# Kernel optimization log

Hardware: AMD Instinct MI355X
Metric: run time of the kernel (lower is better)

Reference implementation:

```python
import jax, jax.numpy as jnp
import numpy as np

N_NODES = 100000
N_EDGES = 1600000
IN_DIM, HID_DIM, OUT_DIM = 64, 64, 16


def setup_inputs() -> dict:
    key = jax.random.key(0)
    k1, k2, k3, k4 = jax.random.split(key, 4)
    x = jax.random.normal(k1, (N_NODES, IN_DIM), dtype=jnp.float32)
    edge_index = jax.random.randint(k2, (2, N_EDGES), 0, N_NODES, dtype=jnp.int64)
    W1 = jax.random.normal(k3, (IN_DIM, HID_DIM), dtype=jnp.float32) * (1.0 / np.sqrt(IN_DIM))
    b1 = jnp.zeros((HID_DIM,), dtype=jnp.float32)
    W2 = jax.random.normal(k4, (HID_DIM, OUT_DIM), dtype=jnp.float32) * (1.0 / np.sqrt(HID_DIM))
    b2 = jnp.zeros((OUT_DIM,), dtype=jnp.float32)
    return {"x": x, "edge_index": edge_index, "W1": W1, "b1": b1, "W2": W2, "b2": b2}


def gcn_conv(x, src, dst, W, b, num_nodes):
    """GCNConv: h = D^{-1/2} (A+I) D^{-1/2} (x W) + b, edge-list form with self-loops already appended."""
    # symmetric degree normalization (degree counted at destination, incl. self-loops)
    deg = jax.ops.segment_sum(jnp.ones_like(dst, dtype=x.dtype), dst, num_segments=num_nodes)
    dinv = jnp.where(deg > 0, jax.lax.rsqrt(deg), 0.0)
    norm = dinv[src] * dinv[dst]                      # [E+N]
    h = x @ W                                         # [N, H] project first (fewer flops on edges)
    msg = h[src] * norm[:, None]                      # gather + scale, [E+N, H]
    out = jax.ops.segment_sum(msg, dst, num_segments=num_nodes)  # scatter-add
    return out + b


def reference(x, edge_index, W1, b1, W2, b2):
    num_nodes = x.shape[0]
    loop = jnp.arange(num_nodes, dtype=edge_index.dtype)
    src = jnp.concatenate([edge_index[0], loop])      # add self-loops once, reuse for both layers
    dst = jnp.concatenate([edge_index[1], loop])
    h = gcn_conv(x, src, dst, W1, b1, num_nodes)
    h = jax.nn.relu(h)
    # F.dropout(training=self.training): eval mode -> identity
    out = gcn_conv(h, src, dst, W2, b2, num_nodes)
    return out
```

## Files before the change

### kernel.cpp

```cpp
#include <hip/hip_runtime.h>

constexpr int N_NODES = 100000;
constexpr int F1 = 64;
constexpr int F2 = 16;
constexpr int SH = 7;
constexpr int NPB = 128;
constexpr int NBINS = (N_NODES + NPB - 1) / NPB;
constexpr int CAPB = 2560;
constexpr int TILE = 4096;

static __device__ __forceinline__ unsigned short f2bf(float f) {
    unsigned int u = __float_as_uint(f);
    unsigned int r = (u + 0x7fffu + ((u >> 16) & 1u)) >> 16;
    return (unsigned short)r;
}
static __device__ __forceinline__ float bf2f(unsigned short b) {
    return __uint_as_float(((unsigned int)b) << 16);
}
static __device__ __forceinline__ float lo16(unsigned int u) { return __uint_as_float(u << 16); }
static __device__ __forceinline__ float hi16(unsigned int u) { return __uint_as_float(u & 0xFFFF0000u); }

__global__ __launch_bounds__(512) void k_bin(const int* __restrict__ src,
                                             const int* __restrict__ dst, int E,
                                             unsigned int* __restrict__ gcnt,
                                             unsigned int* __restrict__ entries) {
    __shared__ unsigned int cnt[NBINS];
    __shared__ unsigned int cur[NBINS];
    int tid = threadIdx.x;
    int base = blockIdx.x * TILE;
    int end = min(base + TILE, E + N_NODES);
    for (int i = tid; i < NBINS; i += 512) cnt[i] = 0;
    __syncthreads();
    for (int e = base + tid; e < end; e += 512) {
        int d = (e < E) ? dst[e] : (e - E);
        atomicAdd(&cnt[d >> SH], 1u);
    }
    __syncthreads();
    for (int i = tid; i < NBINS; i += 512) {
        unsigned int c = cnt[i];
        cur[i] = (unsigned int)i * CAPB + (c ? atomicAdd(&gcnt[i], c) : 0u);
    }
    __syncthreads();
    for (int e = base + tid; e < end; e += 512) {
        int d, s;
        if (e < E) { d = dst[e]; s = src[e]; }
        else       { d = e - E;  s = d; }
        int bb = d >> SH;
        unsigned int p = atomicAdd(&cur[bb], 1u);
        if (p - (unsigned int)bb * CAPB < CAPB)
            entries[p] = (unsigned int)s | ((unsigned int)(d & (NPB - 1)) << 17);
    }
}

__global__ __launch_bounds__(512) void k_csr(const unsigned int* __restrict__ gcnt,
                                             const unsigned int* __restrict__ entries,
                                             uint2* __restrict__ nrange,
                                             unsigned int* __restrict__ sorted,
                                             float* __restrict__ dinv) {
    __shared__ unsigned int ncnt[NPB];
    __shared__ unsigned int noff[NPB + 1];
    __shared__ unsigned int cur[NPB];
    int tid = threadIdx.x;
    int b = blockIdx.x;
    unsigned int cntE = gcnt[b]; if (cntE > CAPB) cntE = CAPB;
    unsigned int base = (unsigned int)b * CAPB;
    if (tid < NPB) ncnt[tid] = 0;
    __syncthreads();
    for (unsigned int e = tid; e < cntE; e += 512)
        atomicAdd(&ncnt[entries[base + e] >> 17], 1u);
    __syncthreads();
    if (tid < NPB) cur[tid] = ncnt[tid];
    __syncthreads();
    for (int ofs = 1; ofs < NPB; ofs <<= 1) {
        unsigned int v = (tid < NPB && tid >= ofs) ? cur[tid - ofs] : 0u;
        __syncthreads();
        if (tid < NPB) cur[tid] += v;
        __syncthreads();
    }
    if (tid < NPB) noff[tid + 1] = cur[tid];
    if (tid == 0) noff[0] = 0;
    __syncthreads();
    if (tid < NPB) {
        int node = b * NPB + tid;
        if (node < N_NODES) {
            dinv[node] = rsqrtf((float)max(ncnt[tid], 1u));
            nrange[node] = make_uint2(base + noff[tid], base + noff[tid + 1]);
        }
        cur[tid] = noff[tid];
    }
    __syncthreads();
    for (unsigned int e = tid; e < cntE; e += 512) {
        unsigned int v = entries[base + e];
        unsigned int p = atomicAdd(&cur[v >> 17], 1u);
        sorted[base + p] = v & 0x1FFFFu;
    }
}

__global__ __launch_bounds__(256) void k_xw1(const float* __restrict__ x,
                                             const float* __restrict__ W,
                                             const float* __restrict__ dinv,
                                             unsigned short* __restrict__ hs) {
    constexpr int XS = 68;
    __shared__ float Ws[64 * 64];
    __shared__ float xs[64 * XS];
    int tid = threadIdx.x;
    int r0 = blockIdx.x * 64;
    for (int i = tid; i < 1024; i += 256) {
        int k = i >> 4, c4 = (i & 15) << 2;
        *(float4*)&Ws[k * 64 + c4] = *(const float4*)&W[k * 64 + c4];
    }
    for (int i = tid; i < 1024; i += 256) {
        int rr = i >> 4, c4 = (i & 15) << 2;
        int r = r0 + rr;
        float4 v = make_float4(0.f, 0.f, 0.f, 0.f);
        if (r < N_NODES) v = *(const float4*)&x[(size_t)r * 64 + c4];
        *(float4*)&xs[rr * XS + c4] = v;
    }
    __syncthreads();
    int tx = tid & 15, ty = tid >> 4;
    int c0 = tx << 2, rb = ty << 2;
    float acc[4][4] = {};
#pragma unroll 8
    for (int k = 0; k < 64; ++k) {
        float4 w = *(float4*)&Ws[k * 64 + c0];
        float x0 = xs[(rb + 0) * XS + k];
        float x1 = xs[(rb + 1) * XS + k];
        float x2 = xs[(rb + 2) * XS + k];
        float x3 = xs[(rb + 3) * XS + k];
        acc[0][0] += x0 * w.x; acc[0][1] += x0 * w.y; acc[0][2] += x0 * w.z; acc[0][3] += x0 * w.w;
        acc[1][0] += x1 * w.x; acc[1][1] += x1 * w.y; acc[1][2] += x1 * w.z; acc[1][3] += x1 * w.w;
        acc[2][0] += x2 * w.x; acc[2][1] += x2 * w.y; acc[2][2] += x2 * w.z; acc[2][3] += x2 * w.w;
        acc[3][0] += x3 * w.x; acc[3][1] += x3 * w.y; acc[3][2] += x3 * w.z; acc[3][3] += x3 * w.w;
    }
#pragma unroll
    for (int i = 0; i < 4; ++i) {
        int r = r0 + rb + i;
        if (r >= N_NODES) break;
        float dv = dinv[r];
        ushort4 p;
        p.x = f2bf(acc[i][0] * dv);
        p.y = f2bf(acc[i][1] * dv);
        p.z = f2bf(acc[i][2] * dv);
        p.w = f2bf(acc[i][3] * dv);
        *(ushort4*)&hs[(size_t)r * 64 + c0] = p;
    }
}

__global__ __launch_bounds__(256) void k_agg1f(const uint2* __restrict__ nrange,
                                               const unsigned int* __restrict__ sorted,
                                               const unsigned short* __restrict__ hs,
                                               const float* __restrict__ dinv,
                                               unsigned short* __restrict__ out1) {
    int gw = (blockIdx.x * 256 + threadIdx.x) >> 6;
    if (gw >= N_NODES) return;
    int lane = threadIdx.x & 63;
    int slot = lane >> 4, t = lane & 15;
    const uint2* hs8 = (const uint2*)hs;
    uint2 rg = nrange[gw];
    float a0 = 0.f, a1 = 0.f, a2 = 0.f, a3 = 0.f;
    for (unsigned int j = rg.x; j < rg.y; j += 64) {
        unsigned int cnt = rg.y - j; if (cnt > 64u) cnt = 64u;
        unsigned int idx = (unsigned)lane < cnt ? sorted[j + lane] : 0u;
        unsigned int rounds = (cnt + 3u) >> 2;
#pragma unroll 4
        for (unsigned int r = 0; r < rounds; ++r) {
            unsigned int sl = (r << 2) + (unsigned)slot;
            unsigned int myidx = (unsigned int)__shfl((int)idx, (int)sl);
            if (sl < cnt) {
                uint2 u = hs8[(size_t)myidx * 16 + t];
                a0 += lo16(u.x); a1 += hi16(u.x);
                a2 += lo16(u.y); a3 += hi16(u.y);
            }
        }
    }
    a0 += __shfl_xor(a0, 16); a1 += __shfl_xor(a1, 16);
    a2 += __shfl_xor(a2, 16); a3 += __shfl_xor(a3, 16);
    a0 += __shfl_xor(a0, 32); a1 += __shfl_xor(a1, 32);
    a2 += __shfl_xor(a2, 32); a3 += __shfl_xor(a3, 32);
    if (slot == 0) {
        float dv = dinv[gw];
        uint2 w;
        w.x = (unsigned)f2bf(a0 * dv) | ((unsigned)f2bf(a1 * dv) << 16);
        w.y = (unsigned)f2bf(a2 * dv) | ((unsigned)f2bf(a3 * dv) << 16);
        ((uint2*)out1)[(size_t)gw * 16 + t] = w;
    }
}

__global__ __launch_bounds__(256) void k_xw2(const unsigned short* __restrict__ out1,
                                             const float* __restrict__ b1,
                                             const float* __restrict__ W2,
                                             const float* __restrict__ dinv,
                                             unsigned short* __restrict__ h2s) {
    constexpr int RS = 66;
    __shared__ float Ws[64 * 16];
    __shared__ float rs[128 * RS];
    __shared__ float b1s[64];
    int tid = threadIdx.x;
    int r0 = blockIdx.x * 128;
    if (tid < 64) b1s[tid] = b1[tid];
    for (int i = tid; i < 256; i += 256)
        *(float4*)&Ws[i * 4] = *(const float4*)&W2[i * 4];
    __syncthreads();
    for (int i = tid; i < 2048; i += 256) {
        int rr = i >> 4, c4 = (i & 15) << 2;
        int r = r0 + rr;
        float v0 = 0.f, v1 = 0.f, v2 = 0.f, v3 = 0.f;
        if (r < N_NODES) {
            ushort4 u = *(const ushort4*)&out1[(size_t)r * 64 + c4];
            v0 = fmaxf(bf2f(u.x) + b1s[c4 + 0], 0.f);
            v1 = fmaxf(bf2f(u.y) + b1s[c4 + 1], 0.f);
            v2 = fmaxf(bf2f(u.z) + b1s[c4 + 2], 0.f);
            v3 = fmaxf(bf2f(u.w) + b1s[c4 + 3], 0.f);
        }
        float* pp = &rs[rr * RS + c4];
        pp[0] = v0; pp[1] = v1; pp[2] = v2; pp[3] = v3;
    }
    __syncthreads();
    int tx = tid & 3, ty = tid >> 2;
    int c0 = tx << 2, rb = ty << 1;
    float acc[2][4] = {};
#pragma unroll 8
    for (int k = 0; k < 64; ++k) {
        float4 w = *(float4*)&Ws[k * 16 + c0];
        float x0 = rs[(rb + 0) * RS + k];
        float x1 = rs[(rb + 1) * RS + k];
        acc[0][0] += x0 * w.x; acc[0][1] += x0 * w.y; acc[0][2] += x0 * w.z; acc[0][3] += x0 * w.w;
        acc[1][0] += x1 * w.x; acc[1][1] += x1 * w.y; acc[1][2] += x1 * w.z; acc[1][3] += x1 * w.w;
    }
#pragma unroll
    for (int i = 0; i < 2; ++i) {
        int r = r0 + rb + i;
        if (r >= N_NODES) break;
        float dv = dinv[r];
        ushort4 p;
        p.x = f2bf(acc[i][0] * dv);
        p.y = f2bf(acc[i][1] * dv);
        p.z = f2bf(acc[i][2] * dv);
        p.w = f2bf(acc[i][3] * dv);
        *(ushort4*)&h2s[(size_t)r * 16 + c0] = p;
    }
}

__global__ __launch_bounds__(256) void k_agg2f(const uint2* __restrict__ nrange,
                                               const unsigned int* __restrict__ sorted,
                                               const unsigned short* __restrict__ h2s,
                                               const float* __restrict__ dinv,
                                               const float* __restrict__ b2,
                                               float* __restrict__ out) {
    int gw = (blockIdx.x * 256 + threadIdx.x) >> 6;
    if (gw >= N_NODES) return;
    int lane = threadIdx.x & 63;
    int slot = lane >> 3, t = lane & 7;
    const unsigned int* h232 = (const unsigned int*)h2s;
    uint2 rg = nrange[gw];
    float a0 = 0.f, a1 = 0.f;
    for (unsigned int j = rg.x; j < rg.y; j += 64) {
        unsigned int cnt = rg.y - j; if (cnt > 64u) cnt = 64u;
        unsigned int idx = (unsigned)lane < cnt ? sorted[j + lane] : 0u;
        unsigned int rounds = (cnt + 7u) >> 3;
#pragma unroll 4
        for (unsigned int r = 0; r < rounds; ++r) {
            unsigned int sl = (r << 3) + (unsigned)slot;
            unsigned int myidx = (unsigned int)__shfl((int)idx, (int)sl);
            if (sl < cnt) {
                unsigned int u = h232[(size_t)myidx * 8 + t];
                a0 += lo16(u);
                a1 += hi16(u);
            }
        }
    }
    a0 += __shfl_xor(a0, 8);  a1 += __shfl_xor(a1, 8);
    a0 += __shfl_xor(a0, 16); a1 += __shfl_xor(a1, 16);
    a0 += __shfl_xor(a0, 32); a1 += __shfl_xor(a1, 32);
    if (slot == 0) {
        float dv = dinv[gw];
        float2 o;
        o.x = a0 * dv + b2[2 * t];
        o.y = a1 * dv + b2[2 * t + 1];
        *(float2*)&out[(size_t)gw * 16 + 2 * t] = o;
    }
}

static inline size_t align256(size_t x) { return (x + 255) & ~size_t(255); }

extern "C" void kernel_launch(void* const* d_in, const int* in_sizes, int n_in,
                              void* d_out, int out_size, void* d_ws, size_t ws_size,
                              hipStream_t stream) {
    const float* x  = (const float*)d_in[0];
    const int* edge = (const int*)d_in[1];
    const float* W1 = (const float*)d_in[2];
    const float* b1 = (const float*)d_in[3];
    const float* W2 = (const float*)d_in[4];
    const float* b2 = (const float*)d_in[5];
    float* out = (float*)d_out;

    const int E = in_sizes[1] / 2;
    const int* src = edge;
    const int* dst = edge + E;

    char* ws = (char*)d_ws;
    size_t o = 0;
    unsigned int* gcnt    = (unsigned int*)(ws + o); o += align256((size_t)NBINS * 4);
    float* dinv           = (float*)(ws + o);        o += align256((size_t)N_NODES * 4);
    unsigned int* entries = (unsigned int*)(ws + o); o += align256((size_t)NBINS * CAPB * 4);
    unsigned int* sorted  = (unsigned int*)(ws + o); o += align256((size_t)NBINS * CAPB * 4);
    uint2* nrange         = (uint2*)(ws + o);        o += align256((size_t)N_NODES * 8);
    unsigned short* hs    = (unsigned short*)(ws + o); o += align256((size_t)N_NODES * F1 * 2);
    unsigned short* out1  = (unsigned short*)(ws + o); o += align256((size_t)N_NODES * F1 * 2);
    unsigned short* h2s   = (unsigned short*)(ws + o); o += align256((size_t)N_NODES * F2 * 2);

    hipMemsetAsync(gcnt, 0, (size_t)NBINS * 4, stream);

    int nbinblocks = (E + N_NODES + TILE - 1) / TILE;
    k_bin<<<nbinblocks, 512, 0, stream>>>(src, dst, E, gcnt, entries);
    k_csr<<<NBINS, 512, 0, stream>>>(gcnt, entries, nrange, sorted, dinv);

    k_xw1<<<(N_NODES + 63) / 64, 256, 0, stream>>>(x, W1, dinv, hs);
    {
        int blocks = (int)(((long long)N_NODES * 64 + 255) / 256);
        k_agg1f<<<blocks, 256, 0, stream>>>(nrange, sorted, hs, dinv, out1);
    }

    k_xw2<<<(N_NODES + 127) / 128, 256, 0, stream>>>(out1, b1, W2, dinv, h2s);
    {
        int blocks = (int)(((long long)N_NODES * 64 + 255) / 256);
        k_agg2f<<<blocks, 256, 0, stream>>>(nrange, sorted, h2s, dinv, b2, out);
    }
}
```

Baseline: 155.2 us.

## Fuse layer-2 projection, bias and ReLU into the layer-1 aggregation kernel

The layer-1 aggregation kernel now applies dinv, bias b1 and ReLU to each aggregated row itself. It stages that row in shared memory and multiplies it by W2 per wavefront, writing the prescaled bf16 h2s directly. This removes the out1 intermediate buffer, its global write and re-read, and the separate k_xw2 launch. In exchange, every block must load the full W2 matrix into shared memory and pass a block-wide barrier first. The per-row 64x16 matvec is done with shuffles rather than a tiled GEMM, and layer-1 outputs are no longer rounded to bf16 before the projection.

```diff
diff --git a/kernel.cpp b/kernel.cpp
--- a/kernel.cpp
+++ b/kernel.cpp
@@ -150,10 +150,20 @@
                                                const unsigned int* __restrict__ sorted,
                                                const unsigned short* __restrict__ hs,
                                                const float* __restrict__ dinv,
-                                               unsigned short* __restrict__ out1) {
-    int gw = (blockIdx.x * 256 + threadIdx.x) >> 6;
+                                               const float* __restrict__ b1,
+                                               const float* __restrict__ W2,
+                                               unsigned short* __restrict__ h2s) {
+    __shared__ float W2s[64 * 17];
+    __shared__ float b1s[64];
+    __shared__ float rowbuf[4][64];
+    int tid = threadIdx.x;
+    for (int i = tid; i < 1024; i += 256) W2s[(i >> 4) * 17 + (i & 15)] = W2[i];
+    if (tid < 64) b1s[tid] = b1[tid];
+    __syncthreads();
+    int gw = (blockIdx.x * 256 + tid) >> 6;
     if (gw >= N_NODES) return;
-    int lane = threadIdx.x & 63;
+    int wv = (tid >> 6) & 3;
+    int lane = tid & 63;
     int slot = lane >> 4, t = lane & 15;
     const uint2* hs8 = (const uint2*)hs;
     uint2 rg = nrange[gw];
@@ -177,68 +187,25 @@
     a2 += __shfl_xor(a2, 16); a3 += __shfl_xor(a3, 16);
     a0 += __shfl_xor(a0, 32); a1 += __shfl_xor(a1, 32);
     a2 += __shfl_xor(a2, 32); a3 += __shfl_xor(a3, 32);
+    float dv = dinv[gw];
     if (slot == 0) {
-        float dv = dinv[gw];
-        uint2 w;
-        w.x = (unsigned)f2bf(a0 * dv) | ((unsigned)f2bf(a1 * dv) << 16);
-        w.y = (unsigned)f2bf(a2 * dv) | ((unsigned)f2bf(a3 * dv) << 16);
-        ((uint2*)out1)[(size_t)gw * 16 + t] = w;
-    }
-}
-
-__global__ __launch_bounds__(256) void k_xw2(const unsigned short* __restrict__ out1,
-                                             const float* __restrict__ b1,
-                                             const float* __restrict__ W2,
-                                             const float* __restrict__ dinv,
-                                             unsigned short* __restrict__ h2s) {
-    constexpr int RS = 66;
-    __shared__ float Ws[64 * 16];
-    __shared__ float rs[128 * RS];
-    __shared__ float b1s[64];
-    int tid = threadIdx.x;
-    int r0 = blockIdx.x * 128;
-    if (tid < 64) b1s[tid] = b1[tid];
-    for (int i = tid; i < 256; i += 256)
-        *(float4*)&Ws[i * 4] = *(const float4*)&W2[i * 4];
-    __syncthreads();
-    for (int i = tid; i < 2048; i += 256) {
-        int rr = i >> 4, c4 = (i & 15) << 2;
-        int r = r0 + rr;
-        float v0 = 0.f, v1 = 0.f, v2 = 0.f, v3 = 0.f;
-        if (r < N_NODES) {
-            ushort4 u = *(const ushort4*)&out1[(size_t)r * 64 + c4];
-            v0 = fmaxf(bf2f(u.x) + b1s[c4 + 0], 0.f);
-            v1 = fmaxf(bf2f(u.y) + b1s[c4 + 1], 0.f);
-            v2 = fmaxf(bf2f(u.z) + b1s[c4 + 2], 0.f);
-            v3 = fmaxf(bf2f(u.w) + b1s[c4 + 3], 0.f);
-        }
-        float* pp = &rs[rr * RS + c4];
-        pp[0] = v0; pp[1] = v1; pp[2] = v2; pp[3] = v3;
-    }
-    __syncthreads();
-    int tx = tid & 3, ty = tid >> 2;
-    int c0 = tx << 2, rb = ty << 1;
-    float acc[2][4] = {};
-#pragma unroll 8
-    for (int k = 0; k < 64; ++k) {
-        float4 w = *(float4*)&Ws[k * 16 + c0];
-        float x0 = rs[(rb + 0) * RS + k];
-        float x1 = rs[(rb + 1) * RS + k];
-        acc[0][0] += x0 * w.x; acc[0][1] += x0 * w.y; acc[0][2] += x0 * w.z; acc[0][3] += x0 * w.w;
-        acc[1][0] += x1 * w.x; acc[1][1] += x1 * w.y; acc[1][2] += x1 * w.z; acc[1][3] += x1 * w.w;
-    }
+        float4 r;
+        r.x = fmaxf(a0 * dv + b1s[4 * t + 0], 0.f);
+        r.y = fmaxf(a1 * dv + b1s[4 * t + 1], 0.f);
+        r.z = fmaxf(a2 * dv + b1s[4 * t + 2], 0.f);
+        r.w = fmaxf(a3 * dv + b1s[4 * t + 3], 0.f);
+        *(float4*)&rowbuf[wv][4 * t] = r;
+    }
+    int c = lane & 15, q = lane >> 4;
+    float s = 0.f;
 #pragma unroll
-    for (int i = 0; i < 2; ++i) {
-        int r = r0 + rb + i;
-        if (r >= N_NODES) break;
-        float dv = dinv[r];
-        ushort4 p;
-        p.x = f2bf(acc[i][0] * dv);
-        p.y = f2bf(acc[i][1] * dv);
-        p.z = f2bf(acc[i][2] * dv);
-        p.w = f2bf(acc[i][3] * dv);
-        *(ushort4*)&h2s[(size_t)r * 16 + c0] = p;
-    }
+    for (int kk = 0; kk < 16; ++kk) {
+        int k = (q << 4) + kk;
+        s += rowbuf[wv][k] * W2s[k * 17 + c];
+    }
+    s += __shfl_xor(s, 16);
+    s += __shfl_xor(s, 32);
+    if (lane < 16) h2s[(size_t)gw * 16 + c] = f2bf(s * dv);
 }
 
 __global__ __launch_bounds__(256) void k_agg2f(const uint2* __restrict__ nrange,
@@ -306,7 +273,6 @@
     unsigned int* sorted  = (unsigned int*)(ws + o); o += align256((size_t)NBINS * CAPB * 4);
     uint2* nrange         = (uint2*)(ws + o);        o += align256((size_t)N_NODES * 8);
     unsigned short* hs    = (unsigned short*)(ws + o); o += align256((size_t)N_NODES * F1 * 2);
-    unsigned short* out1  = (unsigned short*)(ws + o); o += align256((size_t)N_NODES * F1 * 2);
     unsigned short* h2s   = (unsigned short*)(ws + o); o += align256((size_t)N_NODES * F2 * 2);
 
     hipMemsetAsync(gcnt, 0, (size_t)NBINS * 4, stream);
@@ -318,10 +284,9 @@
     k_xw1<<<(N_NODES + 63) / 64, 256, 0, stream>>>(x, W1, dinv, hs);
     {
         int blocks = (int)(((long long)N_NODES * 64 + 255) / 256);
-        k_agg1f<<<blocks, 256, 0, stream>>>(nrange, sorted, hs, dinv, out1);
-    }
-
-    k_xw2<<<(N_NODES + 127) / 128, 256, 0, stream>>>(out1, b1, W2, dinv, h2s);
+        k_agg1f<<<blocks, 256, 0, stream>>>(nrange, sorted, hs, dinv, b1, W2, h2s);
+    }
+
     {
         int blocks = (int)(((long long)N_NODES * 64 + 255) / 256);
         k_agg2f<<<blocks, 256, 0, stream>>>(nrange, sorted, h2s, dinv, b2, out);
```

New measurement: 163.4 us. 5.2% more time.
